# Kernel optimization log

Measured on AMD Instinct MI355X. Metric: run time of the kernel, lower is better.

Reference implementation:

```python
import jax, jax.numpy as jnp
import numpy as np

B, S, HID = 2, 2048, 2048
H, HKV, D = 16, 8, 128
RQ, RK, RV = 6, 2, 2
WINDOW = 1024
SOFTCAP = 50.0
SCALING = D ** -0.5
NEG_INF = -2.3819763e38  # gemma mask fill value (fp32 safe)


def _rope(x, cos, sin):
    # Gemma rotary: split last dim into two halves treated as (real, imag).
    d2 = x.shape[-1] // 2
    x1, x2 = x[..., :d2], x[..., d2:]
    return jnp.concatenate([x1 * cos - x2 * sin, x1 * sin + x2 * cos], axis=-1)


def setup_inputs() -> dict:
    key = jax.random.key(0)
    ks = jax.random.split(key, 8)
    hidden_states = jax.random.normal(ks[0], (B, S, HID), jnp.float32)
    w = 0.02
    W_A_q = jax.random.normal(ks[1], (HID, H * RQ), jnp.float32) * w
    W_B_q = jax.random.normal(ks[2], (HID, H * RQ * D), jnp.float32) * w
    W_A_k = jax.random.normal(ks[3], (HID, HKV * RK), jnp.float32) * w
    W_B_k = jax.random.normal(ks[4], (HID, RK * D), jnp.float32) * w
    W_A_v = jax.random.normal(ks[5], (HID, HKV * RV), jnp.float32) * w
    W_B_v = jax.random.normal(ks[6], (HID, RV * D), jnp.float32) * w
    W_o = jax.random.normal(ks[7], (H * D, HID), jnp.float32) * w
    # rotary tables (theta=10000)
    pos = jnp.arange(S, dtype=jnp.float32)
    inv = 1.0 / (10000.0 ** (jnp.arange(0, D, 2, dtype=jnp.float32) / D))
    ang = pos[:, None] * inv[None, :]  # [S, D/2]
    freqs_cos, freqs_sin = jnp.cos(ang), jnp.sin(ang)
    # causal + sliding-window additive mask [B,1,S,S]
    i = jnp.arange(S)[:, None]
    j = jnp.arange(S)[None, :]
    allowed = (j <= i) & (i - j < WINDOW)
    mask = jnp.where(allowed, 0.0, NEG_INF).astype(jnp.float32)
    mask = jnp.broadcast_to(mask[None, None], (B, 1, S, S))
    kv_write_indices = jnp.arange(S, dtype=jnp.int32)  # prefill: identity write
    return {
        'hidden_states': hidden_states, 'W_A_q': W_A_q, 'W_B_q': W_B_q,
        'W_A_k': W_A_k, 'W_B_k': W_B_k, 'W_A_v': W_A_v, 'W_B_v': W_B_v,
        'W_o': W_o, 'freqs_cos': freqs_cos, 'freqs_sin': freqs_sin,
        'mask': mask, 'kv_write_indices': kv_write_indices,
    }


def reference(hidden_states, W_A_q, W_B_q, W_A_k, W_B_k, W_A_v, W_B_v, W_o,
              freqs_cos, freqs_sin, mask, kv_write_indices):
    # Prefill: kv_write_indices == arange(S); factorized cache == current factors.
    b, s, _ = hidden_states.shape
    Aq = (hidden_states @ W_A_q).reshape(b, s, H, RQ)       # [b,s,H,Rq]
    Bq = (hidden_states @ W_B_q).reshape(b, s, H, RQ, D)    # [b,s,H,Rq,d]
    Ak = (hidden_states @ W_A_k).reshape(b, s, HKV, RK)
    Bk = (hidden_states @ W_B_k).reshape(b, s, RK, D)
    Av = (hidden_states @ W_A_v).reshape(b, s, HKV, RV)
    Bv = (hidden_states @ W_B_v).reshape(b, s, RV, D)
    # RoPE on the B factors (as in the original: applied to B_q rows and B_k rows)
    Bq = _rope(Bq, freqs_cos[:, None, None, :], freqs_sin[:, None, None, :])
    Bk = _rope(Bk, freqs_cos[:, None, :], freqs_sin[:, None, :])
    # Contract rank factors. Identical math to the per-head
    # einsum('bqrd,bksd->bqkrs') + einsum('bqr,bks,bqkrs->bqk') since the
    # bilinear form factorizes: sum_{r,s} Aq_r Ak_s <Bq_r, Bk_s> = <q, k>.
    q = jnp.einsum('bshr,bshrd->bshd', Aq, Bq)               # [b,s,H,d]
    k = jnp.einsum('bsgr,bsrd->bsgd', Ak, Bk)                # [b,s,Hkv,d]
    v = jnp.einsum('bsgr,bsrd->bsgd', Av, Bv)
    rep = H // HKV
    k = jnp.repeat(k, rep, axis=2)                            # GQA expand
    v = jnp.repeat(v, rep, axis=2)
    scores = jnp.einsum('bqhd,bkhd->bhqk', q, k) * SCALING
    scores = jnp.tanh(scores / SOFTCAP) * SOFTCAP             # logit softcap
    scores = scores + mask                                    # local sliding mask
    probs = jax.nn.softmax(scores, axis=-1)
    out = jnp.einsum('bhqk,bkhd->bqhd', probs, v).reshape(b, s, H * D)
    return out @ W_o
```

## Files before the change

kernel.cpp:

```cpp
#include <hip/hip_runtime.h>
#include <hip/hip_bf16.h>

#define S_LEN 2048
#define HID 2048
#define NB 2
#define NH 16
#define NKV 8
#define DH 128
#define RQ 6
#define KG 2048
#define SCALING 0.08838834764831845f

typedef __attribute__((ext_vector_type(8))) short s16x8;
typedef __attribute__((ext_vector_type(4))) float f32x4;

__device__ __forceinline__ float bf2f(ushort u) {
    union { unsigned int i; float f; } v; v.i = ((unsigned int)u) << 16; return v.f;
}
__device__ __forceinline__ ushort f2bf(float f) {
    __hip_bfloat16 h = __float2bfloat16(f);
    return *reinterpret_cast<ushort*>(&h);
}
__device__ __forceinline__ void g2lds16(const void* g, void* l) {
    __builtin_amdgcn_global_load_lds((const __attribute__((address_space(1))) void*)g,
                                     (__attribute__((address_space(3))) void*)l, 16, 0, 0);
}

__global__ void k_prep(const float* __restrict__ hs, const float* __restrict__ WAq,
                       const float* __restrict__ WAk, const float* __restrict__ WAv,
                       const float* __restrict__ WBk, const float* __restrict__ WBv,
                       const float* __restrict__ WBq, const float* __restrict__ Wo,
                       ushort* __restrict__ Xb, ushort* __restrict__ WtS,
                       ushort* __restrict__ WtBq, ushort* __restrict__ WtWo) {
    __shared__ ushort tile[64][68];
    int idx = blockIdx.x;
    int t = threadIdx.x;
    if (idx < 2048) {
#pragma unroll
        for (int j = 0; j < 4; ++j) {
            int i = idx * 1024 + t + j * 256;
            float4 v = ((const float4*)hs)[i];
            ushort4 o;
            o.x = f2bf(v.x); o.y = f2bf(v.y); o.z = f2bf(v.z); o.w = f2bf(v.w);
            ((ushort4*)Xb)[i] = o;
        }
        return;
    }
    idx -= 2048;
    const float* in; ushort* out; int Nin, rowOff;
    if (idx < 64)        { in = WAq; out = WtS;  Nin = 96;    rowOff = 0; }
    else if (idx < 96)   { idx -= 64;   in = WAk; out = WtS;  Nin = 16;    rowOff = 96; }
    else if (idx < 128)  { idx -= 96;   in = WAv; out = WtS;  Nin = 16;    rowOff = 112; }
    else if (idx < 256)  { idx -= 128;  in = WBk; out = WtS;  Nin = 256;   rowOff = 128; }
    else if (idx < 384)  { idx -= 256;  in = WBv; out = WtS;  Nin = 256;   rowOff = 384; }
    else if (idx < 6528) { idx -= 384;  in = WBq; out = WtBq; Nin = 12288; rowOff = 0; }
    else                 { idx -= 6528; in = Wo;  out = WtWo; Nin = 2048;  rowOff = 0; }
    int k0 = (idx & 31) * 64, n0 = (idx >> 5) * 64;
#pragma unroll
    for (int i = 0; i < 4; ++i) {
        int f = t + i * 256;
        int r = f >> 4;
        int c = (f & 15) * 4;
        int nn = n0 + c;
        float4 v = make_float4(0.f, 0.f, 0.f, 0.f);
        if (nn < Nin) v = *(const float4*)&in[(size_t)(k0 + r) * Nin + nn];
        ushort4 u;
        u.x = f2bf(v.x); u.y = f2bf(v.y); u.z = f2bf(v.z); u.w = f2bf(v.w);
        *(ushort4*)&tile[r][c] = u;
    }
    __syncthreads();
#pragma unroll
    for (int i = 0; i < 4; ++i) {
        int f = t + i * 256;
        int nr = f >> 4;
        int kc = (f & 15) * 4;
        int nn = n0 + nr;
        if (nn < Nin) {
            ushort4 u;
            u.x = tile[kc][nr]; u.y = tile[kc + 1][nr];
            u.z = tile[kc + 2][nr]; u.w = tile[kc + 3][nr];
            *(ushort4*)&out[(size_t)(rowOff + nn) * KG + k0 + kc] = u;
        }
    }
}

__device__ __forceinline__ void stc(float* p, float v) { *p = v; }
__device__ __forceinline__ void stc(ushort* p, float v) { *p = f2bf(v); }

template<typename OutT>
__global__ __launch_bounds__(256, 2) void k_gemm(const ushort* __restrict__ A,
                                                 const ushort* __restrict__ Bt,
                                                 OutT* __restrict__ C, int ldc) {
    __shared__ ushort lA[128 * 64];
    __shared__ ushort lB[128 * 64];
    const int tid = threadIdx.x;
    const int l = tid & 63, w = tid >> 6;
    const int gx = gridDim.x;
    int flat = blockIdx.y * gx + blockIdx.x;
    const int nwg = gx * gridDim.y;
    if ((nwg & 7) == 0) {
        int qq = nwg >> 3;
        flat = (flat & 7) * qq + (flat >> 3);
    }
    const int m0 = (flat % gx) * 128, n0 = (flat / gx) * 128;
    const int wm = w >> 1, wn = w & 1;
    f32x4 acc[4][4] = {};
    const int swz = 16 * ((tid & 7) ^ ((tid >> 3) & 7));
    const int rowbase = tid >> 3;

    for (int k0 = 0; k0 < KG; k0 += 64) {
#pragma unroll
        for (int i = 0; i < 4; ++i) {
            int row = rowbase + i * 32;
            const char* srcA = (const char*)A + (((size_t)(m0 + row) * KG + k0) * 2) + swz;
            g2lds16(srcA, (char*)lA + tid * 16 + i * 4096);
            const char* srcB = (const char*)Bt + (((size_t)(n0 + row) * KG + k0) * 2) + swz;
            g2lds16(srcB, (char*)lB + tid * 16 + i * 4096);
        }
        __syncthreads();
#pragma unroll
        for (int kk = 0; kk < 2; ++kk) {
            s16x8 af[4], bfr[4];
            const int kb = kk * 64 + (l >> 4) * 16;
#pragma unroll
            for (int mf = 0; mf < 4; ++mf) {
                int row = wm * 64 + mf * 16 + (l & 15);
                af[mf] = *(const s16x8*)((const char*)lA + row * 128 + (kb ^ ((row & 7) << 4)));
            }
#pragma unroll
            for (int nf = 0; nf < 4; ++nf) {
                int row = wn * 64 + nf * 16 + (l & 15);
                bfr[nf] = *(const s16x8*)((const char*)lB + row * 128 + (kb ^ ((row & 7) << 4)));
            }
#pragma unroll
            for (int mf = 0; mf < 4; ++mf)
#pragma unroll
                for (int nf = 0; nf < 4; ++nf)
                    acc[mf][nf] = __builtin_amdgcn_mfma_f32_16x16x32_bf16(af[mf], bfr[nf], acc[mf][nf], 0, 0, 0);
        }
        __syncthreads();
    }
#pragma unroll
    for (int mf = 0; mf < 4; ++mf)
#pragma unroll
        for (int r = 0; r < 4; ++r) {
            int row = m0 + wm * 64 + mf * 16 + (l >> 4) * 4 + r;
#pragma unroll
            for (int nf = 0; nf < 4; ++nf) {
                int col = n0 + wn * 64 + nf * 16 + (l & 15);
                stc(C + (size_t)row * ldc + col, acc[mf][nf][r]);
            }
        }
}

__global__ __launch_bounds__(512, 2) void k_gemm8(const ushort* __restrict__ A,
                                                  const ushort* __restrict__ Bt,
                                                  ushort* __restrict__ C, int ldc) {
    __shared__ char sB[131072];
    const int tid = threadIdx.x;
    const int l = tid & 63, wid = tid >> 6;
    const int wr = wid >> 2, wc = wid & 3;

    int flat = blockIdx.x;
    const int nwg = gridDim.x;
    if ((nwg & 7) == 0) {
        int qq = nwg >> 3;
        flat = (flat & 7) * qq + (flat >> 3);
    }
    const int m0 = (flat & 15) * 256;
    const int n0 = (flat >> 4) * 256;

    const int rb = tid >> 3;
    const int swz = 16 * ((tid & 7) ^ (rb & 7));
    const char* pAh[2][2];
    const char* pBh[2][2];
#pragma unroll
    for (int h = 0; h < 2; ++h)
#pragma unroll
        for (int j = 0; j < 2; ++j) {
            pAh[h][j] = (const char*)A + (size_t)(m0 + j * 128 + h * 64 + rb) * (KG * 2) + swz;
            pBh[h][j] = (const char*)Bt + (size_t)(n0 + (j * 2 + (tid >> 8)) * 64 + h * 32 + (rb & 31)) * (KG * 2) + swz;
        }

    f32x4 acc[8][4] = {};
    s16x8 af[4][2], bf[4][2];

    const int arow = (l & 15) * 128;
    const int kxor0 = (0 * 64 + (l >> 4) * 16) ^ ((l & 7) << 4);
    const int kxor1 = (1 * 64 + (l >> 4) * 16) ^ ((l & 7) << 4);

#define STG_A(T, D, H)                                                                     \
    do {                                                                                   \
        g2lds16(pAh[H][0] + (size_t)(T) * 128, sB + (D) * 65536 + (H) * 16384 + tid * 16); \
        g2lds16(pAh[H][1] + (size_t)(T) * 128, sB + (D) * 65536 + (H) * 16384 + 8192 + tid * 16); \
    } while (0)
#define STG_B(T, D, H)                                                                     \
    do {                                                                                   \
        g2lds16(pBh[H][0] + (size_t)(T) * 128, sB + (D) * 65536 + 32768 + (H) * 16384 + tid * 16); \
        g2lds16(pBh[H][1] + (size_t)(T) * 128, sB + (D) * 65536 + 32768 + (H) * 16384 + 8192 + tid * 16); \
    } while (0)
#define RD_A(D, MH)                                                                        \
    do {                                                                                   \
        const char* ab = sB + (D) * 65536 + (MH) * 16384 + wr * 8192;                      \
        _Pragma("unroll") for (int mi = 0; mi < 4; ++mi) {                                 \
            af[mi][0] = *(const s16x8*)(ab + mi * 2048 + arow + kxor0);                    \
            af[mi][1] = *(const s16x8*)(ab + mi * 2048 + arow + kxor1);                    \
        }                                                                                  \
    } while (0)
#define RD_B(D, BH)                                                                        \
    do {                                                                                   \
        const char* bb = sB + (D) * 65536 + 32768 + (BH) * 16384 + wc * 4096;              \
        _Pragma("unroll") for (int ni = 0; ni < 2; ++ni) {                                 \
            bf[(BH) * 2 + ni][0] = *(const s16x8*)(bb + ni * 2048 + arow + kxor0);         \
            bf[(BH) * 2 + ni][1] = *(const s16x8*)(bb + ni * 2048 + arow + kxor1);         \
        }                                                                                  \
    } while (0)
#define QMFMA(MQ, NQ)                                                                      \
    do {                                                                                   \
        __builtin_amdgcn_s_setprio(1);                                                     \
        _Pragma("unroll") for (int mi = 0; mi < 4; ++mi)                                   \
        _Pragma("unroll") for (int ni = 0; ni < 2; ++ni)                                   \
        _Pragma("unroll") for (int k2 = 0; k2 < 2; ++k2)                                   \
            acc[(MQ) * 4 + mi][(NQ) * 2 + ni] = __builtin_amdgcn_mfma_f32_16x16x32_bf16(   \
                af[mi][k2], bf[(NQ) * 2 + ni][k2], acc[(MQ) * 4 + mi][(NQ) * 2 + ni], 0, 0, 0); \
        __builtin_amdgcn_s_setprio(0);                                                     \
    } while (0)
#define BAR()                                   \
    do {                                        \
        asm volatile("" ::: "memory");          \
        __builtin_amdgcn_s_barrier();           \
        asm volatile("" ::: "memory");          \
    } while (0)
#define VM6() asm volatile("s_waitcnt vmcnt(6)" ::: "memory")
#define VM0() asm volatile("s_waitcnt vmcnt(0)" ::: "memory")

    STG_A(0, 0, 0); STG_A(0, 0, 1); STG_B(0, 0, 0); STG_B(0, 0, 1);
    STG_B(1, 1, 0); STG_B(1, 1, 1); STG_A(1, 1, 0);
    VM6();
    BAR();

    for (int i = 0; i < 16; ++i) {
        const bool last = (i == 15);
        const int t1 = 2 * i + 1, t2 = 2 * i + 2, t3 = 2 * i + 3;
        RD_A(0, 0); RD_B(0, 0);
        STG_A(t1, 1, 1);
        BAR(); QMFMA(0, 0); BAR();
        RD_B(0, 1);
        if (!last) STG_A(t2, 0, 0);
        BAR(); QMFMA(0, 1); BAR();
        RD_A(0, 1);
        if (!last) STG_B(t2, 0, 0);
        BAR(); QMFMA(1, 1); BAR();
        if (!last) { STG_B(t2, 0, 1); VM6(); } else { VM0(); }
        BAR(); QMFMA(1, 0); BAR();
        RD_A(1, 0); RD_B(1, 0);
        if (!last) STG_A(t2, 0, 1);
        BAR(); QMFMA(0, 0); BAR();
        RD_B(1, 1);
        if (!last) STG_B(t3, 1, 0);
        BAR(); QMFMA(0, 1); BAR();
        RD_A(1, 1);
        if (!last) STG_B(t3, 1, 1);
        BAR(); QMFMA(1, 1); BAR();
        if (!last) { STG_A(t3, 1, 0); VM6(); }
        BAR(); QMFMA(1, 0); BAR();
    }

#undef STG_A
#undef STG_B
#undef RD_A
#undef RD_B
#undef QMFMA

#pragma unroll
    for (int mf = 0; mf < 8; ++mf)
#pragma unroll
        for (int r = 0; r < 4; ++r) {
            int row = m0 + wr * 128 + mf * 16 + (l >> 4) * 4 + r;
#pragma unroll
            for (int nf = 0; nf < 4; ++nf) {
                int col = n0 + wc * 64 + nf * 16 + (l & 15);
                C[(size_t)row * ldc + col] = f2bf(acc[mf][nf][r]);
            }
        }
#undef BAR
#undef VM6
#undef VM0
}

__global__ __launch_bounds__(512, 2) void k_gemm8h(const ushort* __restrict__ A,
                                                   const ushort* __restrict__ Bt,
                                                   float* __restrict__ C, int ldc) {
    __shared__ char sB[98304];
    const int tid = threadIdx.x;
    const int l = tid & 63, wid = tid >> 6;
    const int wr = wid >> 2, wc = wid & 3;

    int flat = blockIdx.x;
    const int nwg = gridDim.x;
    if ((nwg & 7) == 0) {
        int qq = nwg >> 3;
        flat = (flat & 7) * qq + (flat >> 3);
    }
    const int m0 = (flat & 31) * 128;
    const int n0 = (flat >> 5) * 256;

    const int rb = tid >> 3;
    const int swz = 16 * ((tid & 7) ^ (rb & 7));
    const char* pA_[2];
    const char* pB_[2][2];
#pragma unroll
    for (int h = 0; h < 2; ++h) {
        pA_[h] = (const char*)A + (size_t)(m0 + (tid >> 8) * 64 + h * 32 + (rb & 31)) * (KG * 2) + swz;
#pragma unroll
        for (int j = 0; j < 2; ++j)
            pB_[h][j] = (const char*)Bt + (size_t)(n0 + (j * 2 + (tid >> 8)) * 64 + h * 32 + (rb & 31)) * (KG * 2) + swz;
    }

    f32x4 acc[4][4] = {};
    s16x8 af[2][2], bf[4][2];

    const int arow = (l & 15) * 128;
    const int kxor0 = ((l >> 4) * 16) ^ ((l & 7) << 4);
    const int kxor1 = (64 + (l >> 4) * 16) ^ ((l & 7) << 4);

#define STG_AH(T, D, H)                                                                    \
    g2lds16(pA_[H] + (size_t)(T) * 128, sB + (D) * 49152 + (H) * 8192 + tid * 16)
#define STG_BH(T, D, H)                                                                    \
    do {                                                                                   \
        g2lds16(pB_[H][0] + (size_t)(T) * 128, sB + (D) * 49152 + 16384 + (H) * 16384 + tid * 16); \
        g2lds16(pB_[H][1] + (size_t)(T) * 128, sB + (D) * 49152 + 16384 + (H) * 16384 + 8192 + tid * 16); \
    } while (0)
#define RD_AH(D, MH)                                                                       \
    do {                                                                                   \
        const char* ab = sB + (D) * 49152 + (MH) * 8192 + wr * 4096;                       \
        _Pragma("unroll") for (int mi = 0; mi < 2; ++mi) {                                 \
            af[mi][0] = *(const s16x8*)(ab + mi * 2048 + arow + kxor0);                    \
            af[mi][1] = *(const s16x8*)(ab + mi * 2048 + arow + kxor1);                    \
        }                                                                                  \
    } while (0)
#define RD_BH(D, BH)                                                                       \
    do {                                                                                   \
        const char* bb = sB + (D) * 49152 + 16384 + (BH) * 16384 + wc * 4096;              \
        _Pragma("unroll") for (int ni = 0; ni < 2; ++ni) {                                 \
            bf[(BH) * 2 + ni][0] = *(const s16x8*)(bb + ni * 2048 + arow + kxor0);         \
            bf[(BH) * 2 + ni][1] = *(const s16x8*)(bb + ni * 2048 + arow + kxor1);         \
        }                                                                                  \
    } while (0)
#define QMFMAH(MQ, NQ)                                                                     \
    do {                                                                                   \
        __builtin_amdgcn_s_setprio(1);                                                     \
        _Pragma("unroll") for (int mi = 0; mi < 2; ++mi)                                   \
        _Pragma("unroll") for (int ni = 0; ni < 2; ++ni)                                   \
        _Pragma("unroll") for (int k2 = 0; k2 < 2; ++k2)                                   \
            acc[(MQ) * 2 + mi][(NQ) * 2 + ni] = __builtin_amdgcn_mfma_f32_16x16x32_bf16(   \
                af[mi][k2], bf[(NQ) * 2 + ni][k2], acc[(MQ) * 2 + mi][(NQ) * 2 + ni], 0, 0, 0); \
        __builtin_amdgcn_s_setprio(0);                                                     \
    } while (0)
#define BAR()                                   \
    do {                                        \
        asm volatile("" ::: "memory");          \
        __builtin_amdgcn_s_barrier();           \
        asm volatile("" ::: "memory");          \
    } while (0)
#define VM5() asm volatile("s_waitcnt vmcnt(5)" ::: "memory")
#define VM0() asm volatile("s_waitcnt vmcnt(0)" ::: "memory")

    STG_AH(0, 0, 0); STG_AH(0, 0, 1); STG_BH(0, 0, 0); STG_BH(0, 0, 1);
    STG_BH(1, 1, 0); STG_BH(1, 1, 1); STG_AH(1, 1, 0);
    VM5();
    BAR();

    for (int i = 0; i < 16; ++i) {
        const bool last = (i == 15);
        const int t1 = 2 * i + 1, t2 = 2 * i + 2, t3 = 2 * i + 3;
        RD_AH(0, 0); RD_BH(0, 0);
        STG_AH(t1, 1, 1);
        BAR(); QMFMAH(0, 0); BAR();
        RD_BH(0, 1);
        if (!last) STG_AH(t2, 0, 0);
        BAR(); QMFMAH(0, 1); BAR();
        RD_AH(0, 1);
        if (!last) STG_BH(t2, 0, 0);
        BAR(); QMFMAH(1, 1); BAR();
        if (!last) { STG_BH(t2, 0, 1); VM5(); } else { VM0(); }
        BAR(); QMFMAH(1, 0); BAR();
        RD_AH(1, 0); RD_BH(1, 0);
        if (!last) STG_AH(t2, 0, 1);
        BAR(); QMFMAH(0, 0); BAR();
        RD_BH(1, 1);
        if (!last) STG_BH(t3, 1, 0);
        BAR(); QMFMAH(0, 1); BAR();
        RD_AH(1, 1);
        if (!last) STG_BH(t3, 1, 1);
        BAR(); QMFMAH(1, 1); BAR();
        if (!last) { STG_AH(t3, 1, 0); VM5(); }
        BAR(); QMFMAH(1, 0); BAR();
    }

#undef STG_AH
#undef STG_BH
#undef RD_AH
#undef RD_BH
#undef QMFMAH
#undef BAR
#undef VM5
#undef VM0

#pragma unroll
    for (int a = 0; a < 4; ++a)
#pragma unroll
        for (int r = 0; r < 4; ++r) {
            int row = m0 + wr * 64 + a * 16 + (l >> 4) * 4 + r;
#pragma unroll
            for (int b2 = 0; b2 < 4; ++b2) {
                int col = n0 + wc * 64 + b2 * 16 + (l & 15);
                C[(size_t)row * ldc + col] = acc[a][b2][r];
            }
        }
}

__global__ void k_contract_q(const ushort* __restrict__ bq, const float* __restrict__ small,
                             const float* __restrict__ cosT, const float* __restrict__ sinT,
                             ushort* __restrict__ q, int pitch, int hbase) {
    int srow = blockIdx.x;
    int b = srow >> 11, sl = srow & 2047;
    int t = threadIdx.x;
    int l = t & 63;
    int hloc = blockIdx.y * 4 + (t >> 6);
    int h = hbase + hloc;
    const ushort* bqr = bq + (size_t)srow * pitch + hloc * 768;
    const float* af = small + (size_t)srow * 640 + h * RQ;
    float y0 = 0.f, y1 = 0.f;
#pragma unroll
    for (int r = 0; r < RQ; ++r) {
        float a = af[r];
        ushort2 v = *(const ushort2*)&bqr[r * 128 + 2 * l];
        y0 += a * bf2f(v.x);
        y1 += a * bf2f(v.y);
    }
    float z0 = __shfl_xor(y0, 32);
    float z1 = __shfl_xor(y1, 32);
    int d = (l & 31) * 2;
    float2 cs = *(const float2*)&cosT[sl * 64 + d];
    float2 sn = *(const float2*)&sinT[sl * 64 + d];
    size_t o = ((size_t)(b * NH + h) * S_LEN + sl) * DH;
    ushort2 outv;
    if (l < 32) {
        outv.x = f2bf((y0 * cs.x - z0 * sn.x) * SCALING);
        outv.y = f2bf((y1 * cs.y - z1 * sn.y) * SCALING);
        *(ushort2*)&q[o + d] = outv;
    } else {
        outv.x = f2bf((z0 * sn.x + y0 * cs.x) * SCALING);
        outv.y = f2bf((z1 * sn.y + y1 * cs.y) * SCALING);
        *(ushort2*)&q[o + 64 + d] = outv;
    }
}

__global__ void k_contract_kv(const float* __restrict__ small, const float* __restrict__ cosT,
                              const float* __restrict__ sinT, ushort* __restrict__ kk,
                              ushort* __restrict__ vT) {
    int srow = blockIdx.x;
    int b = srow >> 11, sl = srow & 2047;
    int t = threadIdx.x;
    int d2 = t & 63, g = t >> 6;
    const float* row = small + (size_t)srow * 640;
    float k1 = 0.f, k2 = 0.f, v1 = 0.f, v2 = 0.f;
#pragma unroll
    for (int r = 0; r < 2; ++r) {
        float ak = row[96 + g * 2 + r];
        k1 += ak * row[128 + r * 128 + d2];
        k2 += ak * row[128 + r * 128 + 64 + d2];
        float av = row[112 + g * 2 + r];
        v1 += av * row[384 + r * 128 + d2];
        v2 += av * row[384 + r * 128 + 64 + d2];
    }
    float c = cosT[sl * 64 + d2], s = sinT[sl * 64 + d2];
    float kr1 = k1 * c - k2 * s, kr2 = k1 * s + k2 * c;
    size_t ko = ((size_t)(b * NKV + g) * S_LEN + sl) * DH + d2;
    kk[ko] = f2bf(kr1);
    kk[ko + 64] = f2bf(kr2);
    size_t vo = ((size_t)(b * NKV + g) * DH + d2) * S_LEN + sl;
    vT[vo] = f2bf(v1);
    vT[vo + (size_t)64 * S_LEN] = f2bf(v2);
}

__device__ __forceinline__ float softcap_p(float x) {
    float z = x * 0.02f;
    float z2 = z * z;
    float num = z * fmaf(z2, z2 + 105.f, 945.f);
    float den = fmaf(z2, fmaf(z2, 15.f, 420.f), 945.f);
    return __expf(fmaf(50.f, __fdividef(num, den), -50.f));
}

__global__ __launch_bounds__(512, 2) void k_attn(const ushort* __restrict__ q, const ushort* __restrict__ kk,
                                                 const ushort* __restrict__ vT, ushort* __restrict__ O) {
    __shared__ char sK[16384];
    __shared__ char sV[16384];
    __shared__ char sP[16384];
    const int f = blockIdx.x;
    const int xcd = f & 7;
    const int j = f >> 3;
    const int bg = xcd * 2 + (j >> 5);
    const int qb = 31 - (j & 31);
    const int b = bg >> 3, g = bg & 7;
    const int tid = threadIdx.x, l = tid & 63, w = tid >> 6;
    const int w4 = w & 3;
    const int h = g * 2 + (w >> 2);
    const int qs = qb * 64;
    const int q0 = qs + w4 * 16;

    const ushort* qbase = q + ((size_t)(b * NH + h) * S_LEN) * DH;
    s16x8 qf[4];
    {
        const char* qrow = (const char*)(qbase + (size_t)(q0 + (l & 15)) * DH);
#pragma unroll
        for (int ds = 0; ds < 4; ++ds)
            qf[ds] = *(const s16x8*)(qrow + ds * 64 + (l >> 4) * 16);
    }
    f32x4 acc[8] = {};
    float lrow[4] = {0.f, 0.f, 0.f, 0.f};

    const size_t kgbase = ((size_t)(b * NKV + g) * S_LEN) * DH * 2;
    const size_t vgbase = ((size_t)(b * NKV + g) * DH) * S_LEN * 2;

    const int jt0 = (qs > 1023) ? ((qs - 1023) >> 6) : 0;
    const int ibase = q0 + (l >> 4) * 4;

    for (int jt = jt0; jt <= qb; ++jt) {
#pragma unroll
        for (int i = 0; i < 2; ++i) {
            int row = (tid >> 4) + i * 32;
            int colb = (tid & 15) * 16;
            const char* src = (const char*)kk + kgbase + ((size_t)(jt * 64 + row)) * 256 + (colb ^ ((row & 7) << 4));
            g2lds16(src, sK + tid * 16 + i * 8192);
        }
#pragma unroll
        for (int i = 0; i < 2; ++i) {
            int row = (tid >> 3) + i * 64;
            int colb = (tid & 7) * 16;
            const char* src = (const char*)vT + vgbase + (size_t)row * 4096 + (size_t)jt * 128 + (colb ^ ((row & 7) << 4));
            g2lds16(src, sV + tid * 16 + i * 8192);
        }
        __syncthreads();

        const bool diag = (jt == qb);
        const bool wclip = (jt == jt0) && (qs > 1023);

        f32x4 sc[4] = {};
#pragma unroll
        for (int ct = 0; ct < 4; ++ct) {
            if (diag && ct > w4) continue;
            f32x4 z = {};
            int row = ct * 16 + (l & 15);
#pragma unroll
            for (int ds = 0; ds < 4; ++ds) {
                int kb = ds * 64 + (l >> 4) * 16;
                s16x8 kf = *(const s16x8*)(sK + row * 256 + (kb ^ ((row & 7) << 4)));
                z = __builtin_amdgcn_mfma_f32_16x16x32_bf16(qf[ds], kf, z, 0, 0, 0);
            }
            sc[ct] = z;
        }
        float p[4][4];
        if (!diag && !wclip) {
#pragma unroll
            for (int ct = 0; ct < 4; ++ct)
#pragma unroll
                for (int r = 0; r < 4; ++r) {
                    float pe = softcap_p(sc[ct][r]);
                    p[ct][r] = pe;
                    lrow[r] += pe;
                }
        } else if (diag) {
#pragma unroll
            for (int ct = 0; ct < 4; ++ct) {
                if (ct > w4) {
#pragma unroll
                    for (int r = 0; r < 4; ++r) p[ct][r] = 0.f;
                    continue;
                }
                int j2 = jt * 64 + ct * 16 + (l & 15);
#pragma unroll
                for (int r = 0; r < 4; ++r) {
                    float pe = softcap_p(sc[ct][r]);
                    pe = (j2 <= ibase + r) ? pe : 0.f;
                    p[ct][r] = pe;
                    lrow[r] += pe;
                }
            }
        } else {
#pragma unroll
            for (int ct = 0; ct < 4; ++ct) {
                int j2 = jt * 64 + ct * 16 + (l & 15);
#pragma unroll
                for (int r = 0; r < 4; ++r) {
                    float pe = softcap_p(sc[ct][r]);
                    pe = (j2 > ibase + r - 1024) ? pe : 0.f;
                    p[ct][r] = pe;
                    lrow[r] += pe;
                }
            }
        }
#pragma unroll
        for (int ct = 0; ct < 4; ++ct) {
            int col = ct * 16 + (l & 15);
#pragma unroll
            for (int r = 0; r < 4; ++r) {
                int row = (l >> 4) * 4 + r;
                *(ushort*)(sP + w * 2048 + row * 128 + ((col * 2) ^ ((row & 7) << 4))) = f2bf(p[ct][r]);
            }
        }
#pragma unroll
        for (int s2 = 0; s2 < 2; ++s2) {
            int rowp = l & 15;
            int kb = s2 * 64 + (l >> 4) * 16;
            s16x8 pf = *(const s16x8*)(sP + w * 2048 + rowp * 128 + (kb ^ ((rowp & 7) << 4)));
#pragma unroll
            for (int dt = 0; dt < 8; ++dt) {
                int d = dt * 16 + (l & 15);
                s16x8 vf = *(const s16x8*)(sV + d * 128 + (kb ^ ((d & 7) << 4)));
                acc[dt] = __builtin_amdgcn_mfma_f32_16x16x32_bf16(pf, vf, acc[dt], 0, 0, 0);
            }
        }
        __syncthreads();
    }
#pragma unroll
    for (int r = 0; r < 4; ++r) {
        float rs = lrow[r];
        rs += __shfl_xor(rs, 1); rs += __shfl_xor(rs, 2);
        rs += __shfl_xor(rs, 4); rs += __shfl_xor(rs, 8);
        lrow[r] = rs;
    }
#pragma unroll
    for (int r = 0; r < 4; ++r) {
        int row = qs + w4 * 16 + (l >> 4) * 4 + r;
        float inv = 1.f / lrow[r];
#pragma unroll
        for (int dt = 0; dt < 8; ++dt)
            O[((size_t)(b * S_LEN + row)) * HID + h * DH + dt * 16 + (l & 15)] = f2bf(acc[dt][r] * inv);
    }
}

extern "C" void kernel_launch(void* const* d_in, const int* in_sizes, int n_in,
                              void* d_out, int out_size, void* d_ws, size_t ws_size,
                              hipStream_t stream) {
    (void)in_sizes; (void)n_in; (void)out_size;
    const float* hs  = (const float*)d_in[0];
    const float* WAq = (const float*)d_in[1];
    const float* WBq = (const float*)d_in[2];
    const float* WAk = (const float*)d_in[3];
    const float* WBk = (const float*)d_in[4];
    const float* WAv = (const float*)d_in[5];
    const float* WBv = (const float*)d_in[6];
    const float* Wo  = (const float*)d_in[7];
    const float* fc  = (const float*)d_in[8];
    const float* fs  = (const float*)d_in[9];

    char* ws = (char*)d_ws;
    ushort* Xb    = (ushort*)(ws + 0);
    ushort* WtS   = (ushort*)(ws + 16777216);
    ushort* WtBq  = (ushort*)(ws + 19398656);
    ushort* WtWo  = (ushort*)(ws + 69730304);
    float*  Small = (float*) (ws + 78118912);
    ushort* BqC   = (ushort*)(ws + 88604672);

    const bool bigws = (ws_size >= 239599616ull);
    size_t tail = bigws ? 189267968ull : 113770496ull;
    ushort* qB  = (ushort*)(ws + tail);
    ushort* kB  = (ushort*)(ws + tail + 16777216);
    ushort* vTB = (ushort*)(ws + tail + 25165824);
    ushort* OB  = (ushort*)(ws + tail + 33554432);

    k_prep<<<9600, 256, 0, stream>>>(hs, WAq, WAk, WAv, WBk, WBv, WBq, Wo,
                                     Xb, WtS, WtBq, WtWo);

    k_gemm<float><<<dim3(32, 5), 256, 0, stream>>>(Xb, WtS, Small, 640);
    k_contract_kv<<<4096, 512, 0, stream>>>(Small, fc, fs, kB, vTB);

    if (bigws) {
        k_gemm8<<<768, 512, 0, stream>>>(Xb, WtBq, BqC, 12288);
        k_contract_q<<<dim3(4096, 4), 256, 0, stream>>>(BqC, Small, fc, fs, qB, 12288, 0);
    } else {
        for (int c = 0; c < 4; ++c) {
            k_gemm8<<<192, 512, 0, stream>>>(Xb, WtBq + (size_t)c * 3072 * KG, BqC, 3072);
            k_contract_q<<<dim3(4096, 1), 256, 0, stream>>>(BqC, Small, fc, fs, qB, 3072, c * 4);
        }
    }

    k_attn<<<512, 512, 0, stream>>>(qB, kB, vTB, OB);

    k_gemm8h<<<256, 512, 0, stream>>>(OB, WtWo, (float*)d_out, 2048);
}
```

Before: 433.0 us.

## Replace 256x256 Bq GEMM with simpler 256x128 double-buffered kernel

The large Bq projection GEMM drops its 256x256 tile, 128 KB LDS, heavily interleaved quarter-step pipeline and replaces it with a 256x128 tile. The new kernel uses a 32-wide K step, a simple two-stage LDS double buffer (48 KB) and launch bounds allowing 4 blocks per CU, with twice as many workgroups. The aim is higher occupancy and more blocks across the CUs so latency is hidden by other waves rather than by hand scheduling. In exchange, each tile reuses loaded data less, total global traffic rises, and there are twice as many barrier and wait points per K element.

Measured after the change: 466.5 us. +7.7%, slower.

```diff
diff --git a/kernel.cpp b/kernel.cpp
--- a/kernel.cpp
+++ b/kernel.cpp
@@ -153,13 +153,13 @@
         }
 }
 
-__global__ __launch_bounds__(512, 2) void k_gemm8(const ushort* __restrict__ A,
-                                                  const ushort* __restrict__ Bt,
-                                                  ushort* __restrict__ C, int ldc) {
-    __shared__ char sB[131072];
+__global__ __launch_bounds__(512, 4) void k_gemm8v2(const ushort* __restrict__ A,
+                                                    const ushort* __restrict__ Bt,
+                                                    ushort* __restrict__ C, int ldc) {
+    __shared__ char sB[49152];
     const int tid = threadIdx.x;
     const int l = tid & 63, wid = tid >> 6;
-    const int wr = wid >> 2, wc = wid & 3;
+    const int wr = wid >> 1, wc = wid & 1;
 
     int flat = blockIdx.x;
     const int nwg = gridDim.x;
@@ -168,124 +168,70 @@
         flat = (flat & 7) * qq + (flat >> 3);
     }
     const int m0 = (flat & 15) * 256;
-    const int n0 = (flat >> 4) * 256;
-
-    const int rb = tid >> 3;
-    const int swz = 16 * ((tid & 7) ^ (rb & 7));
-    const char* pAh[2][2];
-    const char* pBh[2][2];
-#pragma unroll
-    for (int h = 0; h < 2; ++h)
-#pragma unroll
-        for (int j = 0; j < 2; ++j) {
-            pAh[h][j] = (const char*)A + (size_t)(m0 + j * 128 + h * 64 + rb) * (KG * 2) + swz;
-            pBh[h][j] = (const char*)Bt + (size_t)(n0 + (j * 2 + (tid >> 8)) * 64 + h * 32 + (rb & 31)) * (KG * 2) + swz;
-        }
-
-    f32x4 acc[8][4] = {};
-    s16x8 af[4][2], bf[4][2];
-
-    const int arow = (l & 15) * 128;
-    const int kxor0 = (0 * 64 + (l >> 4) * 16) ^ ((l & 7) << 4);
-    const int kxor1 = (1 * 64 + (l >> 4) * 16) ^ ((l & 7) << 4);
-
-#define STG_A(T, D, H)                                                                     \
-    do {                                                                                   \
-        g2lds16(pAh[H][0] + (size_t)(T) * 128, sB + (D) * 65536 + (H) * 16384 + tid * 16); \
-        g2lds16(pAh[H][1] + (size_t)(T) * 128, sB + (D) * 65536 + (H) * 16384 + 8192 + tid * 16); \
+    const int n0 = (flat >> 4) * 128;
+
+    const int r4 = tid >> 2;
+    const int swzA = (((tid & 3) ^ (r4 & 3)) << 4);
+    const char* pA0 = (const char*)A + (size_t)(m0 + r4) * (KG * 2) + swzA;
+    const char* pA1 = (const char*)A + (size_t)(m0 + 128 + r4) * (KG * 2) + swzA;
+    const char* pB0 = (const char*)Bt + (size_t)(n0 + r4) * (KG * 2) + swzA;
+
+    f32x4 acc[4][4] = {};
+    const int kxorA = (((l >> 4) ^ (l & 3)) << 4);
+    const int arow = (l & 15) * 64;
+
+#define STG2(T, D)                                                         \
+    do {                                                                   \
+        g2lds16(pA0 + (size_t)(T) * 64, sB + (D) * 24576 + tid * 16);      \
+        g2lds16(pA1 + (size_t)(T) * 64, sB + (D) * 24576 + 8192 + tid * 16); \
+        g2lds16(pB0 + (size_t)(T) * 64, sB + (D) * 24576 + 16384 + tid * 16); \
     } while (0)
-#define STG_B(T, D, H)                                                                     \
-    do {                                                                                   \
-        g2lds16(pBh[H][0] + (size_t)(T) * 128, sB + (D) * 65536 + 32768 + (H) * 16384 + tid * 16); \
-        g2lds16(pBh[H][1] + (size_t)(T) * 128, sB + (D) * 65536 + 32768 + (H) * 16384 + 8192 + tid * 16); \
-    } while (0)
-#define RD_A(D, MH)                                                                        \
-    do {                                                                                   \
-        const char* ab = sB + (D) * 65536 + (MH) * 16384 + wr * 8192;                      \
-        _Pragma("unroll") for (int mi = 0; mi < 4; ++mi) {                                 \
-            af[mi][0] = *(const s16x8*)(ab + mi * 2048 + arow + kxor0);                    \
-            af[mi][1] = *(const s16x8*)(ab + mi * 2048 + arow + kxor1);                    \
-        }                                                                                  \
-    } while (0)
-#define RD_B(D, BH)                                                                        \
-    do {                                                                                   \
-        const char* bb = sB + (D) * 65536 + 32768 + (BH) * 16384 + wc * 4096;              \
-        _Pragma("unroll") for (int ni = 0; ni < 2; ++ni) {                                 \
-            bf[(BH) * 2 + ni][0] = *(const s16x8*)(bb + ni * 2048 + arow + kxor0);         \
-            bf[(BH) * 2 + ni][1] = *(const s16x8*)(bb + ni * 2048 + arow + kxor1);         \
-        }                                                                                  \
-    } while (0)
-#define QMFMA(MQ, NQ)                                                                      \
-    do {                                                                                   \
-        __builtin_amdgcn_s_setprio(1);                                                     \
-        _Pragma("unroll") for (int mi = 0; mi < 4; ++mi)                                   \
-        _Pragma("unroll") for (int ni = 0; ni < 2; ++ni)                                   \
-        _Pragma("unroll") for (int k2 = 0; k2 < 2; ++k2)                                   \
-            acc[(MQ) * 4 + mi][(NQ) * 2 + ni] = __builtin_amdgcn_mfma_f32_16x16x32_bf16(   \
-                af[mi][k2], bf[(NQ) * 2 + ni][k2], acc[(MQ) * 4 + mi][(NQ) * 2 + ni], 0, 0, 0); \
-        __builtin_amdgcn_s_setprio(0);                                                     \
-    } while (0)
-#define BAR()                                   \
+#define BAR2()                                  \
     do {                                        \
         asm volatile("" ::: "memory");          \
         __builtin_amdgcn_s_barrier();           \
         asm volatile("" ::: "memory");          \
     } while (0)
-#define VM6() asm volatile("s_waitcnt vmcnt(6)" ::: "memory")
-#define VM0() asm volatile("s_waitcnt vmcnt(0)" ::: "memory")
-
-    STG_A(0, 0, 0); STG_A(0, 0, 1); STG_B(0, 0, 0); STG_B(0, 0, 1);
-    STG_B(1, 1, 0); STG_B(1, 1, 1); STG_A(1, 1, 0);
-    VM6();
-    BAR();
-
-    for (int i = 0; i < 16; ++i) {
-        const bool last = (i == 15);
-        const int t1 = 2 * i + 1, t2 = 2 * i + 2, t3 = 2 * i + 3;
-        RD_A(0, 0); RD_B(0, 0);
-        STG_A(t1, 1, 1);
-        BAR(); QMFMA(0, 0); BAR();
-        RD_B(0, 1);
-        if (!last) STG_A(t2, 0, 0);
-        BAR(); QMFMA(0, 1); BAR();
-        RD_A(0, 1);
-        if (!last) STG_B(t2, 0, 0);
-        BAR(); QMFMA(1, 1); BAR();
-        if (!last) { STG_B(t2, 0, 1); VM6(); } else { VM0(); }
-        BAR(); QMFMA(1, 0); BAR();
-        RD_A(1, 0); RD_B(1, 0);
-        if (!last) STG_A(t2, 0, 1);
-        BAR(); QMFMA(0, 0); BAR();
-        RD_B(1, 1);
-        if (!last) STG_B(t3, 1, 0);
-        BAR(); QMFMA(0, 1); BAR();
-        RD_A(1, 1);
-        if (!last) STG_B(t3, 1, 1);
-        BAR(); QMFMA(1, 1); BAR();
-        if (!last) { STG_A(t3, 1, 0); VM6(); }
-        BAR(); QMFMA(1, 0); BAR();
-    }
-
-#undef STG_A
-#undef STG_B
-#undef RD_A
-#undef RD_B
-#undef QMFMA
-
-#pragma unroll
-    for (int mf = 0; mf < 8; ++mf)
+
+    STG2(0, 0);
+    asm volatile("s_waitcnt vmcnt(0)" ::: "memory");
+    BAR2();
+
+    for (int kt = 0; kt < 64; ++kt) {
+        const int cur = kt & 1;
+        const char* abase = sB + cur * 24576 + wr * 4096 + arow + kxorA;
+        const char* bbase = sB + cur * 24576 + 16384 + wc * 4096 + arow + kxorA;
+        s16x8 af[4], bf[4];
+#pragma unroll
+        for (int mi = 0; mi < 4; ++mi) af[mi] = *(const s16x8*)(abase + mi * 1024);
+#pragma unroll
+        for (int ni = 0; ni < 4; ++ni) bf[ni] = *(const s16x8*)(bbase + ni * 1024);
+        if (kt < 63) STG2(kt + 1, cur ^ 1);
+        BAR2();
+        __builtin_amdgcn_s_setprio(1);
+#pragma unroll
+        for (int mi = 0; mi < 4; ++mi)
+#pragma unroll
+            for (int ni = 0; ni < 4; ++ni)
+                acc[mi][ni] = __builtin_amdgcn_mfma_f32_16x16x32_bf16(af[mi], bf[ni], acc[mi][ni], 0, 0, 0);
+        __builtin_amdgcn_s_setprio(0);
+        if (kt < 63) asm volatile("s_waitcnt vmcnt(0)" ::: "memory");
+        BAR2();
+    }
+#undef STG2
+#undef BAR2
+
+#pragma unroll
+    for (int mi = 0; mi < 4; ++mi)
 #pragma unroll
         for (int r = 0; r < 4; ++r) {
-            int row = m0 + wr * 128 + mf * 16 + (l >> 4) * 4 + r;
-#pragma unroll
-            for (int nf = 0; nf < 4; ++nf) {
-                int col = n0 + wc * 64 + nf * 16 + (l & 15);
-                C[(size_t)row * ldc + col] = f2bf(acc[mf][nf][r]);
-            }
-        }
-#undef BAR
-#undef VM6
-#undef VM0
+            int row = m0 + wr * 64 + mi * 16 + (l >> 4) * 4 + r;
+#pragma unroll
+            for (int ni = 0; ni < 4; ++ni) {
+                int col = n0 + wc * 64 + ni * 16 + (l & 15);
+                C[(size_t)row * ldc + col] = f2bf(acc[mi][ni][r]);
+            }
+        }
 }
 
 __global__ __launch_bounds__(512, 2) void k_gemm8h(const ushort* __restrict__ A,
@@ -678,11 +624,11 @@
     k_contract_kv<<<4096, 512, 0, stream>>>(Small, fc, fs, kB, vTB);
 
     if (bigws) {
-        k_gemm8<<<768, 512, 0, stream>>>(Xb, WtBq, BqC, 12288);
+        k_gemm8v2<<<1536, 512, 0, stream>>>(Xb, WtBq, BqC, 12288);
         k_contract_q<<<dim3(4096, 4), 256, 0, stream>>>(BqC, Small, fc, fs, qB, 12288, 0);
     } else {
         for (int c = 0; c < 4; ++c) {
-            k_gemm8<<<192, 512, 0, stream>>>(Xb, WtBq + (size_t)c * 3072 * KG, BqC, 3072);
+            k_gemm8v2<<<384, 512, 0, stream>>>(Xb, WtBq + (size_t)c * 3072 * KG, BqC, 3072);
             k_contract_q<<<dim3(4096, 1), 256, 0, stream>>>(BqC, Small, fc, fs, qB, 3072, c * 4);
         }
     }
```
